# Kernel optimization log

Measured on AMD Instinct MI355X. Metric: run time of the kernel, lower is better.

Reference implementation:

```python
import jax, jax.numpy as jnp
import numpy as np

N_NODES = 100000
N_EDGES = 1600000
IN_FEATS = 256
OUT_FEATS = 64


def setup_inputs() -> dict:
    key = jax.random.key(0)
    k1, k2, k3, k4 = jax.random.split(key, 4)
    feat = jax.random.normal(k1, (N_NODES, IN_FEATS), dtype=jnp.float32)
    # Glorot uniform init for weight
    limit = float(np.sqrt(6.0 / (IN_FEATS + OUT_FEATS)))
    weight = jax.random.uniform(k2, (IN_FEATS, OUT_FEATS), dtype=jnp.float32,
                                minval=-limit, maxval=limit)
    bias = jnp.zeros((OUT_FEATS,), dtype=jnp.float32)
    src = jax.random.randint(k3, (N_EDGES,), 0, N_NODES, dtype=jnp.int32)
    dst = jax.random.randint(k4, (N_EDGES,), 0, N_NODES, dtype=jnp.int32)
    return {"feat": feat, "weight": weight, "bias": bias, "src": src, "dst": dst}


def reference(feat, weight, bias, src, dst):
    N = feat.shape[0]
    ones = jnp.ones(src.shape[0], dtype=feat.dtype)
    # degrees for symmetric ('both') GCN normalization, clamped to >= 1
    deg_out = jnp.maximum(jax.ops.segment_sum(ones, src, num_segments=N), 1.0)
    deg_in = jnp.maximum(jax.ops.segment_sum(ones, dst, num_segments=N), 1.0)
    norm_out = jax.lax.rsqrt(deg_out)  # [N]
    norm_in = jax.lax.rsqrt(deg_in)    # [N]
    # in_feats > out_feats: project first, then aggregate (forward's taken branch)
    h = jnp.matmul(feat, weight) * norm_out[:, None]          # [N, out]
    agg = jax.ops.segment_sum(h[src], dst, num_segments=N)    # gather+scatter SpMM
    rst = agg * norm_in[:, None] + bias
    return jax.nn.relu(rst)
```

## Files before the change

kernel.cpp:

```cpp
#include <hip/hip_runtime.h>

#define N_NODES 100000
#define N_EDGES 1600000
#define IN_F 256
#define OUT_F 64
#define NPAD 100096
#define NB 391
#define NBLK 200
#define CHUNK 8000
#define MSIZE (2*NB*NBLK)
#define SC_BLOCKS 612
#define CAP 12288

typedef __attribute__((ext_vector_type(8))) _Float16 half8v;
typedef __attribute__((ext_vector_type(4))) float f32x4;

__device__ __forceinline__ unsigned short f2bf(float f) {
    unsigned u = __builtin_bit_cast(unsigned, f);
    return (unsigned short)((u + 0x7FFFu + ((u >> 16) & 1u)) >> 16);
}
__device__ __forceinline__ float bf2f(unsigned s) {
    return __builtin_bit_cast(float, s << 16);
}
__device__ __forceinline__ half8v cvt8(float4 x, float4 y) {
    half8v r;
    r[0] = (_Float16)x.x; r[1] = (_Float16)x.y; r[2] = (_Float16)x.z; r[3] = (_Float16)x.w;
    r[4] = (_Float16)y.x; r[5] = (_Float16)y.y; r[6] = (_Float16)y.z; r[7] = (_Float16)y.w;
    return r;
}

__global__ __launch_bounds__(256) void histA_kernel(const int* __restrict__ src,
                                                    const int* __restrict__ dst,
                                                    int* __restrict__ hist_g,
                                                    const float* __restrict__ W,
                                                    _Float16* __restrict__ Wt2) {
    __shared__ int hD[NB], hS[NB];
    int b = blockIdx.x, t = threadIdx.x;
    if (b < 64) {
        int i = b * 256 + t;
        int k = i >> 6, c = i & 63;
        int ks4 = k >> 5, kin = k & 31, l4v = kin >> 3, kq = kin & 7;
        int cf  = c >> 4, l15v = c & 15;
        size_t idx = (((size_t)(ks4 * 4 + cf) * 64) + l4v * 16 + l15v) * 8 + kq;
        Wt2[idx] = (_Float16)W[i];
    }
    for (int j = t; j < NB; j += 256) { hD[j] = 0; hS[j] = 0; }
    __syncthreads();
    int e0 = b * CHUNK;
    for (int e = e0 + t; e < e0 + CHUNK; e += 256) {
        atomicAdd(&hD[dst[e] >> 8], 1);
        atomicAdd(&hS[src[e] >> 8], 1);
    }
    __syncthreads();
    for (int j = t; j < NB; j += 256) {
        hist_g[j * NBLK + b] = hD[j];
        hist_g[NB * NBLK + j * NBLK + b] = hS[j];
    }
}

__global__ __launch_bounds__(256) void scan1_kernel(int* __restrict__ data,
                                                    int* __restrict__ partials) {
    __shared__ int sm[256];
    int i = blockIdx.x * 256 + threadIdx.x;
    int v = (i < MSIZE) ? data[i] : 0;
    sm[threadIdx.x] = v;
    __syncthreads();
    int x = v;
    #pragma unroll
    for (int off = 1; off < 256; off <<= 1) {
        int tv = 0;
        if ((int)threadIdx.x >= off) tv = sm[threadIdx.x - off];
        __syncthreads();
        x += tv;
        sm[threadIdx.x] = x;
        __syncthreads();
    }
    if (i < MSIZE) data[i] = x - v;
    if (threadIdx.x == 255) partials[blockIdx.x] = x;
}

__global__ __launch_bounds__(1024) void scan2_kernel(int* __restrict__ partials) {
    __shared__ int sm[1024];
    int i = threadIdx.x;
    int v = (i < SC_BLOCKS) ? partials[i] : 0;
    sm[i] = v;
    __syncthreads();
    int x = v;
    #pragma unroll
    for (int off = 1; off < 1024; off <<= 1) {
        int tv = 0;
        if (i >= off) tv = sm[i - off];
        __syncthreads();
        x += tv;
        sm[i] = x;
        __syncthreads();
    }
    if (i < SC_BLOCKS) partials[i] = x - v;
}

__device__ __forceinline__ int gscan(const int* __restrict__ hist_g,
                                     const int* __restrict__ partials, int idx) {
    return hist_g[idx] + partials[idx >> 8];
}

__global__ __launch_bounds__(256) void part_kernel(const int* __restrict__ src,
                                                   const int* __restrict__ dst,
                                                   const int* __restrict__ hist_g,
                                                   const int* __restrict__ partials,
                                                   unsigned* __restrict__ edge_buf,
                                                   int* __restrict__ src_part) {
    __shared__ int curD[NB], curS[NB];
    int b = blockIdx.x, t = threadIdx.x;
    for (int j = t; j < NB; j += 256) {
        curD[j] = gscan(hist_g, partials, j * NBLK + b);
        curS[j] = gscan(hist_g, partials, NB * NBLK + j * NBLK + b) - N_EDGES;
    }
    __syncthreads();
    int e0 = b * CHUNK;
    for (int e = e0 + t; e < e0 + CHUNK; e += 256) {
        int s = src[e], d = dst[e];
        int pD = atomicAdd(&curD[d >> 8], 1);
        edge_buf[pD] = ((unsigned)(d & 255) << 17) | (unsigned)s;
        int pS = atomicAdd(&curS[s >> 8], 1);
        src_part[pS] = s;
    }
}

__global__ __launch_bounds__(256) void bucket_kernel(unsigned* __restrict__ edge_buf,
                                                     const int* __restrict__ hist_g,
                                                     const int* __restrict__ partials,
                                                     int* __restrict__ row_ptr,
                                                     const int* __restrict__ src_part,
                                                     float* __restrict__ norm_out) {
    __shared__ unsigned stage[CAP];
    __shared__ int hist[256];
    __shared__ int cur[256];
    int j = blockIdx.x, t = threadIdx.x;
    int b0 = gscan(hist_g, partials, j * NBLK);
    int b1 = (j + 1 < NB) ? gscan(hist_g, partials, (j + 1) * NBLK) : N_EDGES;
    int cnt = b1 - b0;
    hist[t] = 0;
    __syncthreads();
    for (int i = t; i < cnt; i += 256) {
        unsigned p = edge_buf[b0 + i];
        stage[i] = p;
        atomicAdd(&hist[p >> 17], 1);
    }
    __syncthreads();
    int v = hist[t];
    cur[t] = v;
    __syncthreads();
    int x = v;
    #pragma unroll
    for (int off = 1; off < 256; off <<= 1) {
        int tv = (t >= off) ? cur[t - off] : 0;
        __syncthreads();
        x += tv;
        cur[t] = x;
        __syncthreads();
    }
    int excl = x - v;
    row_ptr[j * 256 + t] = b0 + excl;
    cur[t] = excl;
    __syncthreads();
    for (int i = t; i < cnt; i += 256) {
        unsigned p = stage[i];
        int pos = atomicAdd(&cur[p >> 17], 1);
        edge_buf[b0 + pos] = p & 0x1FFFFu;
    }
    __syncthreads();
    hist[t] = 0;
    __syncthreads();
    int s0 = gscan(hist_g, partials, NB * NBLK + j * NBLK) - N_EDGES;
    int s1 = (j + 1 < NB) ? gscan(hist_g, partials, NB * NBLK + (j + 1) * NBLK) - N_EDGES
                          : N_EDGES;
    for (int e = s0 + t; e < s1; e += 256)
        atomicAdd(&hist[src_part[e] & 255], 1);
    __syncthreads();
    int node = j * 256 + t;
    if (node < N_NODES) {
        int d = hist[t]; if (d < 1) d = 1;
        norm_out[node] = rsqrtf((float)d);
    }
}

__global__ __launch_bounds__(256) void gemm_kernel(const float* __restrict__ feat,
                                                   const _Float16* __restrict__ Wt2,
                                                   const float* __restrict__ norm_out,
                                                   unsigned short* __restrict__ h) {
    __shared__ _Float16 Bs[16384];
    const int tid  = threadIdx.x;
    const int wave = tid >> 6, lane = tid & 63;
    const int l15  = lane & 15, l4 = lane >> 4;
    const int rw0  = blockIdx.x * 128 + wave * 32;

    #pragma unroll
    for (int i = 0; i < 8; ++i) {
        const int fr = i * 4 + wave;
        const _Float16* gsrc = Wt2 + ((size_t)fr * 64 + lane) * 8;
        _Float16* ldst = &Bs[(size_t)fr * 64 * 8];
        __builtin_amdgcn_global_load_lds(
            (const __attribute__((address_space(1))) void*)gsrc,
            (__attribute__((address_space(3))) void*)ldst, 16, 0, 0);
    }

    int r0 = rw0 + l15;
    int r1 = r0 + 16;
    int r0c = r0 < N_NODES ? r0 : 0;
    int r1c = r1 < N_NODES ? r1 : 0;
    const float* pA0 = feat + (size_t)r0c * IN_F + l4 * 8;
    const float* pA1 = feat + (size_t)r1c * IN_F + l4 * 8;

    f32x4 acc[2][4];
    #pragma unroll
    for (int rf = 0; rf < 2; ++rf)
        #pragma unroll
        for (int cf = 0; cf < 4; ++cf)
            acc[rf][cf] = (f32x4){0.f, 0.f, 0.f, 0.f};

    float4 nx0 = *(const float4*)(pA0);
    float4 ny0 = *(const float4*)(pA0 + 4);
    float4 nx1 = *(const float4*)(pA1);
    float4 ny1 = *(const float4*)(pA1 + 4);

    __syncthreads();

    #pragma unroll
    for (int ks4 = 0; ks4 < 8; ++ks4) {
        float4 cx0 = nx0, cy0 = ny0, cx1 = nx1, cy1 = ny1;
        if (ks4 < 7) {
            nx0 = *(const float4*)(pA0 + 32 * (ks4 + 1));
            ny0 = *(const float4*)(pA0 + 32 * (ks4 + 1) + 4);
            nx1 = *(const float4*)(pA1 + 32 * (ks4 + 1));
            ny1 = *(const float4*)(pA1 + 32 * (ks4 + 1) + 4);
        }
        half8v bfr[4];
        #pragma unroll
        for (int cf = 0; cf < 4; ++cf)
            bfr[cf] = *(const half8v*)&Bs[(((size_t)(ks4 * 4 + cf) * 64) + lane) * 8];
        half8v a0 = cvt8(cx0, cy0);
        half8v a1 = cvt8(cx1, cy1);
        #pragma unroll
        for (int cf = 0; cf < 4; ++cf) {
            acc[0][cf] = __builtin_amdgcn_mfma_f32_16x16x32_f16(a0, bfr[cf], acc[0][cf], 0, 0, 0);
            acc[1][cf] = __builtin_amdgcn_mfma_f32_16x16x32_f16(a1, bfr[cf], acc[1][cf], 0, 0, 0);
        }
    }

    #pragma unroll
    for (int rf = 0; rf < 2; ++rf) {
        #pragma unroll
        for (int r = 0; r < 4; ++r) {
            int row = rw0 + rf * 16 + l4 * 4 + r;
            if (row < N_NODES) {
                float s = norm_out[row];
                #pragma unroll
                for (int cf = 0; cf < 4; ++cf)
                    h[(size_t)row * OUT_F + cf * 16 + l15] = f2bf(acc[rf][cf][r] * s);
            }
        }
    }
}

__global__ __launch_bounds__(256) void agg_kernel(const int* __restrict__ row_ptr,
                                                  const unsigned* __restrict__ edge_src,
                                                  const unsigned short* __restrict__ h,
                                                  const float* __restrict__ bias,
                                                  float* __restrict__ out) {
    int wid  = (blockIdx.x * 256 + threadIdx.x) >> 6;
    int lane = threadIdx.x & 63;
    if (wid >= N_NODES) return;
    int g  = lane >> 3;
    int fp = lane & 7;
    int start = row_ptr[wid];
    int end   = row_ptr[wid + 1];
    int deg   = end - start;

    float a[8];
    #pragma unroll
    for (int i = 0; i < 8; ++i) a[i] = 0.f;

    int ecur = start + g;
    int id = (ecur < end) ? (int)edge_src[ecur] : -1;
    for (int e = start; e < end; e += 8) {
        int enext = e + 8 + g;
        int idn = (enext < end) ? (int)edge_src[enext] : -1;
        int s = id >= 0 ? id : 0;
        uint4 w = *(const uint4*)&h[(size_t)s * OUT_F + fp * 8];
        if (id < 0) { w.x = 0u; w.y = 0u; w.z = 0u; w.w = 0u; }
        a[0] += bf2f(w.x & 0xFFFFu); a[1] += bf2f(w.x >> 16);
        a[2] += bf2f(w.y & 0xFFFFu); a[3] += bf2f(w.y >> 16);
        a[4] += bf2f(w.z & 0xFFFFu); a[5] += bf2f(w.z >> 16);
        a[6] += bf2f(w.w & 0xFFFFu); a[7] += bf2f(w.w >> 16);
        id = idn;
    }

    #pragma unroll
    for (int off = 8; off < 64; off <<= 1) {
        #pragma unroll
        for (int i = 0; i < 8; ++i) a[i] += __shfl_xor(a[i], off);
    }

    if (g == 0) {
        int dc = deg < 1 ? 1 : deg;
        float nrm = rsqrtf((float)dc);
        float4 b0 = *(const float4*)&bias[fp * 8];
        float4 b1 = *(const float4*)&bias[fp * 8 + 4];
        float4 r0, r1;
        r0.x = fmaxf(a[0] * nrm + b0.x, 0.f);
        r0.y = fmaxf(a[1] * nrm + b0.y, 0.f);
        r0.z = fmaxf(a[2] * nrm + b0.z, 0.f);
        r0.w = fmaxf(a[3] * nrm + b0.w, 0.f);
        r1.x = fmaxf(a[4] * nrm + b1.x, 0.f);
        r1.y = fmaxf(a[5] * nrm + b1.y, 0.f);
        r1.z = fmaxf(a[6] * nrm + b1.z, 0.f);
        r1.w = fmaxf(a[7] * nrm + b1.w, 0.f);
        *(float4*)&out[(size_t)wid * OUT_F + fp * 8]     = r0;
        *(float4*)&out[(size_t)wid * OUT_F + fp * 8 + 4] = r1;
    }
}

extern "C" void kernel_launch(void* const* d_in, const int* in_sizes, int n_in,
                              void* d_out, int out_size, void* d_ws, size_t ws_size,
                              hipStream_t stream) {
    const float* feat = (const float*)d_in[0];
    const float* W    = (const float*)d_in[1];
    const float* bias = (const float*)d_in[2];
    const int*   src  = (const int*)d_in[3];
    const int*   dst  = (const int*)d_in[4];
    float* out = (float*)d_out;

    char* w = (char*)d_ws;
    size_t off = 0;
    auto take = [&](size_t bytes) { char* p = w + off; off += (bytes + 255) & ~(size_t)255; return p; };

    int*            hist_g   = (int*)take((size_t)MSIZE * 4);
    int*            partials = (int*)take((size_t)SC_BLOCKS * 4);
    float*          norm_out = (float*)take((size_t)NPAD * 4);
    int*            row_ptr  = (int*)take((size_t)(NPAD + 64) * 4);
    _Float16*       Wt2      = (_Float16*)take((size_t)IN_F * OUT_F * 2);
    unsigned*       edge_buf = (unsigned*)take((size_t)N_EDGES * 4);
    unsigned short* h        = (unsigned short*)take((size_t)NPAD * OUT_F * 2);
    int*            src_part = (int*)take((size_t)N_EDGES * 4);

    histA_kernel<<<NBLK, 256, 0, stream>>>(src, dst, hist_g, W, Wt2);
    scan1_kernel<<<SC_BLOCKS, 256, 0, stream>>>(hist_g, partials);
    scan2_kernel<<<1, 1024, 0, stream>>>(partials);
    part_kernel<<<NBLK, 256, 0, stream>>>(src, dst, hist_g, partials, edge_buf, src_part);
    bucket_kernel<<<NB, 256, 0, stream>>>(edge_buf, hist_g, partials, row_ptr, src_part, norm_out);
    gemm_kernel<<<(NPAD / 128), 256, 0, stream>>>(feat, Wt2, norm_out, h);
    agg_kernel<<<(N_NODES * 64 + 255) / 256, 256, 0, stream>>>(row_ptr, edge_buf, h, bias, out);
}
```

Measured before the change: 138.0 us.

## Stage partition writes through shared memory for coalesced bucketed scatter

```diff
diff --git a/kernel.cpp b/kernel.cpp
--- a/kernel.cpp
+++ b/kernel.cpp
@@ -6,10 +6,10 @@
 #define OUT_F 64
 #define NPAD 100096
 #define NB 391
-#define NBLK 200
-#define CHUNK 8000
+#define NBLK 512
+#define CHUNK 3125
 #define MSIZE (2*NB*NBLK)
-#define SC_BLOCKS 612
+#define SC_BLOCKS 1564
 #define CAP 12288
 
 typedef __attribute__((ext_vector_type(8))) _Float16 half8v;
@@ -82,20 +82,23 @@
 __global__ __launch_bounds__(1024) void scan2_kernel(int* __restrict__ partials) {
     __shared__ int sm[1024];
     int i = threadIdx.x;
-    int v = (i < SC_BLOCKS) ? partials[i] : 0;
-    sm[i] = v;
-    __syncthreads();
-    int x = v;
+    int v0 = (2 * i     < SC_BLOCKS) ? partials[2 * i]     : 0;
+    int v1 = (2 * i + 1 < SC_BLOCKS) ? partials[2 * i + 1] : 0;
+    int pv = v0 + v1;
+    sm[i] = pv;
+    __syncthreads();
+    int x = pv;
     #pragma unroll
     for (int off = 1; off < 1024; off <<= 1) {
-        int tv = 0;
-        if (i >= off) tv = sm[i - off];
+        int tv = (i >= off) ? sm[i - off] : 0;
         __syncthreads();
         x += tv;
         sm[i] = x;
         __syncthreads();
     }
-    if (i < SC_BLOCKS) partials[i] = x - v;
+    int excl = x - pv;
+    if (2 * i     < SC_BLOCKS) partials[2 * i]     = excl;
+    if (2 * i + 1 < SC_BLOCKS) partials[2 * i + 1] = excl + v0;
 }
 
 __device__ __forceinline__ int gscan(const int* __restrict__ hist_g,
@@ -109,20 +112,95 @@
                                                    const int* __restrict__ partials,
                                                    unsigned* __restrict__ edge_buf,
                                                    int* __restrict__ src_part) {
-    __shared__ int curD[NB], curS[NB];
-    int b = blockIdx.x, t = threadIdx.x;
+    __shared__ unsigned stageA[CHUNK], stageB[CHUNK];
+    __shared__ int L[512], cur[512];
+    __shared__ int baseD[NB], baseS[NB];
+    const int b = blockIdx.x, t = threadIdx.x;
+    const int e0 = b * CHUNK;
+
     for (int j = t; j < NB; j += 256) {
-        curD[j] = gscan(hist_g, partials, j * NBLK + b);
-        curS[j] = gscan(hist_g, partials, NB * NBLK + j * NBLK + b) - N_EDGES;
-    }
-    __syncthreads();
-    int e0 = b * CHUNK;
-    for (int e = e0 + t; e < e0 + CHUNK; e += 256) {
-        int s = src[e], d = dst[e];
-        int pD = atomicAdd(&curD[d >> 8], 1);
-        edge_buf[pD] = ((unsigned)(d & 255) << 17) | (unsigned)s;
-        int pS = atomicAdd(&curS[s >> 8], 1);
-        src_part[pS] = s;
+        baseD[j] = gscan(hist_g, partials, j * NBLK + b);
+        baseS[j] = gscan(hist_g, partials, NB * NBLK + j * NBLK + b) - N_EDGES;
+    }
+
+    L[t] = 0; L[t + 256] = 0;
+    __syncthreads();
+    for (int i = t; i < CHUNK; i += 256) {
+        int d = dst[e0 + i];
+        stageA[i] = (unsigned)d;
+        atomicAdd(&L[d >> 8], 1);
+    }
+    __syncthreads();
+    int v0 = L[t], v1 = L[t + 256];
+    #pragma unroll
+    for (int off = 1; off < 512; off <<= 1) {
+        int a0 = (t >= off) ? L[t - off] : 0;
+        int a1 = (t + 256 >= off) ? L[t + 256 - off] : 0;
+        __syncthreads();
+        L[t] += a0; L[t + 256] += a1;
+        __syncthreads();
+    }
+    {
+        int i0 = L[t], i1 = L[t + 256];
+        __syncthreads();
+        L[t] = i0 - v0;  L[t + 256] = i1 - v1;
+        cur[t] = i0 - v0; cur[t + 256] = i1 - v1;
+    }
+    __syncthreads();
+    for (int i = t; i < CHUNK; i += 256) {
+        int d = (int)stageA[i];
+        int s = src[e0 + i];
+        stageA[i] = (unsigned)s;
+        int pos = atomicAdd(&cur[d >> 8], 1);
+        stageB[pos] = ((unsigned)(d & 255) << 17) | (unsigned)s;
+    }
+    __syncthreads();
+    for (int i = t; i < CHUNK; i += 256) {
+        int lo = 0, hi = 511;
+        #pragma unroll
+        for (int it = 0; it < 9; ++it) {
+            int mid = (lo + hi + 1) >> 1;
+            if (L[mid] <= i) lo = mid; else hi = mid - 1;
+        }
+        edge_buf[baseD[lo] + (i - L[lo])] = stageB[i];
+    }
+    __syncthreads();
+
+    L[t] = 0; L[t + 256] = 0;
+    __syncthreads();
+    for (int i = t; i < CHUNK; i += 256)
+        atomicAdd(&L[stageA[i] >> 8], 1);
+    __syncthreads();
+    v0 = L[t]; v1 = L[t + 256];
+    #pragma unroll
+    for (int off = 1; off < 512; off <<= 1) {
+        int a0 = (t >= off) ? L[t - off] : 0;
+        int a1 = (t + 256 >= off) ? L[t + 256 - off] : 0;
+        __syncthreads();
+        L[t] += a0; L[t + 256] += a1;
+        __syncthreads();
+    }
+    {
+        int i0 = L[t], i1 = L[t + 256];
+        __syncthreads();
+        L[t] = i0 - v0;  L[t + 256] = i1 - v1;
+        cur[t] = i0 - v0; cur[t + 256] = i1 - v1;
+    }
+    __syncthreads();
+    for (int i = t; i < CHUNK; i += 256) {
+        unsigned s = stageA[i];
+        int pos = atomicAdd(&cur[s >> 8], 1);
+        stageB[pos] = s;
+    }
+    __syncthreads();
+    for (int i = t; i < CHUNK; i += 256) {
+        int lo = 0, hi = 511;
+        #pragma unroll
+        for (int it = 0; it < 9; ++it) {
+            int mid = (lo + hi + 1) >> 1;
+            if (L[mid] <= i) lo = mid; else hi = mid - 1;
+        }
+        src_part[baseS[lo] + (i - L[lo])] = (int)stageB[i];
     }
 }
 
```

After: 135.6 us. About the same (-1.7%).
